# Performance work log

Measured on AMD Instinct MI355X. Metric: run time of the kernel, lower is better.

The kernel has to match this reference:

```python
import jax, jax.numpy as jnp
import numpy as np

B = 2048      # batch (number of event graphs)
NU = 128      # nodes in 'upstream' star graph per sample
ND = 128      # nodes in 'downstream' star graph per sample
FEAT = 10     # raw feature columns; fp[:, :7] used, column -3 (=7) is split flag
IN_DIM = 7    # state_dim + 1 + 2
HID = 64      # hidden1
TAU = 22      # tau_num
ALPHA = 0.2


def star_adj(n):
    # prepare_eg: edges[0,:]=1, symmetrized, diagonal zeroed -> star graph around node 0
    idx = jnp.arange(n)
    return (((idx[:, None] == 0) | (idx[None, :] == 0)) & (idx[:, None] != idx[None, :])).astype(jnp.float32)


def gat(h, W, a, adj, concat):
    # pyGAT GraphAttentionLayer (dropout=0): h [B,n,f], W [f,d], a [2d,1]
    d = W.shape[1]
    Wh = jnp.einsum('bnf,fd->bnd', h, W)                      # [B,n,d]
    e = Wh @ a[:d] + jnp.swapaxes(Wh @ a[d:], 1, 2)           # [B,n,n]
    e = jax.nn.leaky_relu(e, ALPHA)
    e = jnp.where(adj > 0, e, -9e15)
    att = jax.nn.softmax(e, axis=-1)
    hp = jnp.einsum('bnm,bmd->bnd', att, Wh)                  # [B,n,d]
    return jax.nn.elu(hp) if concat else hp


def setup_inputs() -> dict:
    key = jax.random.key(0)
    ks = jax.random.split(key, 12)
    fp = jax.random.normal(ks[0], (B, NU + ND, FEAT), dtype=jnp.float32)
    # column -3: first NU rows negative (u side), last ND rows positive (d side)
    fp = fp.at[:, :NU, FEAT - 3].set(-1.0)
    fp = fp.at[:, NU:, FEAT - 3].set(1.0)
    s = 0.1
    return {
        'fp': fp,
        'u_att_W': jax.random.normal(ks[1], (IN_DIM, HID), jnp.float32) * s,
        'u_att_a': jax.random.normal(ks[2], (2 * HID, 1), jnp.float32) * s,
        'u_out_W': jax.random.normal(ks[3], (HID, HID), jnp.float32) * s,
        'u_out_a': jax.random.normal(ks[4], (2 * HID, 1), jnp.float32) * s,
        'd_att_W': jax.random.normal(ks[5], (IN_DIM, HID), jnp.float32) * s,
        'd_att_a': jax.random.normal(ks[6], (2 * HID, 1), jnp.float32) * s,
        'd_out_W': jax.random.normal(ks[7], (HID, HID), jnp.float32) * s,
        'd_out_a': jax.random.normal(ks[8], (2 * HID, 1), jnp.float32) * s,
        'fc2_W': jax.random.normal(ks[9], (HID, TAU), jnp.float32) * s,
        'fc2_b': jax.random.normal(ks[10], (TAU,), jnp.float32) * s,
    }


def reference(fp, u_att_W, u_att_a, u_out_W, u_out_a,
              d_att_W, d_att_a, d_out_W, d_out_a, fc2_W, fc2_b):
    # static split by the sign of column -3 (fp is constructed so the first NU
    # rows have flag<=0 and the last ND rows have flag>=0, matching prepare_eg)
    u_x = fp[:, :NU, :IN_DIM]   # [B,NU,7]
    d_x = fp[:, NU:, :IN_DIM]   # [B,ND,7]
    u_adj = star_adj(NU)
    d_adj = star_adj(ND)
    # u_egat: 1 attention head (concat->elu) then out layer (no elu), sum over nodes
    u_h = gat(gat(u_x, u_att_W, u_att_a, u_adj, True), u_out_W, u_out_a, u_adj, False)
    u_g = jnp.sum(u_h, axis=1)  # [B,HID]
    d_h = gat(gat(d_x, d_att_W, d_att_a, d_adj, True), d_out_W, d_out_a, d_adj, False)
    d_g = jnp.sum(d_h, axis=1)  # [B,HID]
    a = jax.nn.relu((u_g + d_g) @ fc2_W + fc2_b)  # [B,TAU]
    # torch.sort result is discarded; forward returns W.clamp(0, 10)
    return jnp.clip(a, 0.0, 10.0)
```

## Files before the change

kernel.cpp:

```cpp
#include <hip/hip_runtime.h>
#include <math.h>

#define NB     2048
#define FEAT   10
#define IN_DIM 7
#define HID    64
#define TAU    22
#define ALPHA  0.2f

template <int CTRL>
__device__ __forceinline__ float dpp_mv(float x) {
    return __int_as_float(__builtin_amdgcn_update_dpp(
        0, __float_as_int(x), CTRL, 0xf, 0xf, true));
}

__device__ __forceinline__ float wave_sum64(float v) {
    v += dpp_mv<0xB1>(v);
    v += dpp_mv<0x4E>(v);
    v += dpp_mv<0x141>(v);
    v += dpp_mv<0x140>(v);
    v += dpp_mv<0x142>(v);
    v += dpp_mv<0x143>(v);
    return __int_as_float(__builtin_amdgcn_readlane(__float_as_int(v), 63));
}

__global__ __launch_bounds__(256) void gat_star_one(
    const float* __restrict__ fp,
    const float* __restrict__ uW1, const float* __restrict__ uA1,
    const float* __restrict__ uW2,
    const float* __restrict__ dW1, const float* __restrict__ dA1,
    const float* __restrict__ dW2,
    const float* __restrict__ fcW, const float* __restrict__ fcB,
    float* __restrict__ out)
{
    __shared__ float svs[4][16];
    __shared__ float vvs[4][HID];
    __shared__ float pts[4][HID];
    __shared__ float rrs[4][TAU];

    const int tid  = threadIdx.x;
    const int wave = tid >> 6;
    const int lane = tid & 63;
    const int it   = wave >> 1;
    const int half = wave & 1;
    const int item = blockIdx.x * 2 + it;

    const float* xbase = fp + (size_t)item * 256 * FEAT + half * 128 * FEAT;
    const float* pAp = xbase + lane * FEAT;
    const float* pBp = pAp + 64 * FEAT;
    const float2 a0 = *(const float2*)(pAp + 0);
    const float2 a1 = *(const float2*)(pAp + 2);
    const float2 a2 = *(const float2*)(pAp + 4);
    const float  a6 = pAp[6];
    const float2 b0 = *(const float2*)(pBp + 0);
    const float2 b1 = *(const float2*)(pBp + 2);
    const float2 b2 = *(const float2*)(pBp + 4);
    const float  b6 = pBp[6];
    const float4 x03 = *(const float4*)xbase;
    const float2 x45 = *(const float2*)(xbase + 4);
    const float  x6  = xbase[6];

    const float* W1 = half ? dW1 : uW1;
    const float* A1 = half ? dA1 : uA1;
    float w1c[IN_DIM];
    #pragma unroll
    for (int f = 0; f < IN_DIM; ++f) w1c[f] = W1[f * HID + lane];

    if (lane < 14) {
        const int sp = (lane >= IN_DIM) ? 1 : 0;
        const int f  = lane - sp * IN_DIM;
        const float* wr = W1 + f * HID;
        const float* av = A1 + sp * HID;
        float s0 = 0.f, s1 = 0.f, s2 = 0.f, s3 = 0.f;
        #pragma unroll
        for (int k = 0; k < HID; k += 4) {
            s0 = fmaf(wr[k + 0], av[k + 0], s0);
            s1 = fmaf(wr[k + 1], av[k + 1], s1);
            s2 = fmaf(wr[k + 2], av[k + 2], s2);
            s3 = fmaf(wr[k + 3], av[k + 3], s3);
        }
        svs[wave][sp * 8 + f] = (s0 + s1) + (s2 + s3);
    }
    __builtin_amdgcn_wave_barrier();

    float x0[IN_DIM], xA[IN_DIM], xB[IN_DIM];
    x0[0] = x03.x; x0[1] = x03.y; x0[2] = x03.z; x0[3] = x03.w;
    x0[4] = x45.x; x0[5] = x45.y; x0[6] = x6;
    xA[0] = a0.x; xA[1] = a0.y; xA[2] = a1.x; xA[3] = a1.y;
    xA[4] = a2.x; xA[5] = a2.y; xA[6] = a6;
    xB[0] = b0.x; xB[1] = b0.y; xB[2] = b1.x; xB[3] = b1.y;
    xB[4] = b2.x; xB[5] = b2.y; xB[6] = b6;

    float sv1[IN_DIM], sv2[IN_DIM];
    #pragma unroll
    for (int f = 0; f < IN_DIM; ++f) {
        sv1[f] = svs[wave][f];
        sv2[f] = svs[wave][8 + f];
    }

    float s1 = 0.f, sA = 0.f, sB = 0.f;
    #pragma unroll
    for (int f = 0; f < IN_DIM; ++f) {
        s1 = fmaf(x0[f], sv1[f], s1);
        sA = fmaf(xA[f], sv2[f], sA);
        sB = fmaf(xB[f], sv2[f], sB);
    }
    float eA = s1 + sA; eA = (eA >= 0.f) ? eA : ALPHA * eA;
    float eB = s1 + sB; eB = (eB >= 0.f) ? eB : ALPHA * eB;

    const float qA = (lane == 0) ? 0.f : __expf(eA);
    const float qB = __expf(eB);
    float c[8];
    #pragma unroll
    for (int f = 0; f < IN_DIM; ++f)
        c[f] = wave_sum64(fmaf(qA, xA[f], qB * xB[f]));
    c[7] = wave_sum64(qA + qB);
    const float inv = 1.0f / c[7];

    float h0 = 0.f, h1 = 0.f;
    #pragma unroll
    for (int f = 0; f < IN_DIM; ++f) {
        h0 = fmaf(c[f],  w1c[f], h0);
        h1 = fmaf(x0[f], w1c[f], h1);
    }
    h0 *= inv;
    h0 = (h0 > 0.f) ? h0 : (__expf(h0) - 1.f);
    h1 = (h1 > 0.f) ? h1 : (__expf(h1) - 1.f);
    vvs[wave][lane] = h1 + 127.f * h0;
    __builtin_amdgcn_wave_barrier();

    {
        const float* W2 = half ? dW2 : uW2;
        const float* v  = vvs[wave];
        float t0 = 0.f, t1 = 0.f, t2 = 0.f, t3 = 0.f;
        #pragma unroll
        for (int k = 0; k < HID; k += 4) {
            t0 = fmaf(v[k + 0], W2[(k + 0) * HID + lane], t0);
            t1 = fmaf(v[k + 1], W2[(k + 1) * HID + lane], t1);
            t2 = fmaf(v[k + 2], W2[(k + 2) * HID + lane], t2);
            t3 = fmaf(v[k + 3], W2[(k + 3) * HID + lane], t3);
        }
        pts[wave][lane] = (t0 + t1) + (t2 + t3);
    }
    __builtin_amdgcn_wave_barrier();

    {
        const float* p = pts[wave];
        int t = lane & 31; if (t > TAU - 1) t = TAU - 1;
        const int jb = lane & 32;
        float s0 = 0.f, s1_ = 0.f;
        #pragma unroll
        for (int jj = 0; jj < 32; jj += 2) {
            s0  = fmaf(p[jb + jj],     fcW[(jb + jj)     * TAU + t], s0);
            s1_ = fmaf(p[jb + jj + 1], fcW[(jb + jj + 1) * TAU + t], s1_);
        }
        float s = s0 + s1_;
        s += __shfl_xor(s, 32);
        if (lane < TAU) rrs[wave][lane] = s;
    }
    __syncthreads();

    if (half == 0 && lane < TAU) {
        float s = rrs[wave][lane] + rrs[wave + 1][lane] + fcB[lane];
        s = fminf(fmaxf(s, 0.f), 10.f);
        out[(size_t)item * TAU + lane] = s;
    }
}

extern "C" void kernel_launch(void* const* d_in, const int* in_sizes, int n_in,
                              void* d_out, int out_size, void* d_ws, size_t ws_size,
                              hipStream_t stream) {
    const float* fp  = (const float*)d_in[0];
    const float* uW1 = (const float*)d_in[1];
    const float* uA1 = (const float*)d_in[2];
    const float* uW2 = (const float*)d_in[3];
    const float* dW1 = (const float*)d_in[5];
    const float* dA1 = (const float*)d_in[6];
    const float* dW2 = (const float*)d_in[7];
    const float* fcW = (const float*)d_in[9];
    const float* fcB = (const float*)d_in[10];
    float* out = (float*)d_out;

    gat_star_one<<<NB / 2, 256, 0, stream>>>(fp, uW1, uA1, uW2,
                                             dW1, dA1, dW2, fcW, fcB, out);
}
```

Measured before the change: 16.09 us.

## Replace per-lane serial dot products with wave-parallel DPP reductions and split-k matvecs

Attention-vector projections (W1·a) were computed serially on 14 lanes through shared memory. They are now computed across all lanes with DPP wave reductions. The W2 matvec is restructured as split-k over four 16-lane rows using float4 weight loads plus cross-row shuffles. The fc2 projection is fused directly from registers with row-level DPP sums, which removes the intermediate shared buffer and its barrier. This trades long serial dependent load chains for more cross-lane reduction instructions.

```diff
diff --git a/kernel.cpp b/kernel.cpp
--- a/kernel.cpp
+++ b/kernel.cpp
@@ -14,11 +14,16 @@
         0, __float_as_int(x), CTRL, 0xf, 0xf, true));
 }
 
-__device__ __forceinline__ float wave_sum64(float v) {
+__device__ __forceinline__ float row_sum16(float v) {
     v += dpp_mv<0xB1>(v);
     v += dpp_mv<0x4E>(v);
     v += dpp_mv<0x141>(v);
     v += dpp_mv<0x140>(v);
+    return v;
+}
+
+__device__ __forceinline__ float wave_sum64(float v) {
+    v = row_sum16(v);
     v += dpp_mv<0x142>(v);
     v += dpp_mv<0x143>(v);
     return __int_as_float(__builtin_amdgcn_readlane(__float_as_int(v), 63));
@@ -33,9 +38,7 @@
     const float* __restrict__ fcW, const float* __restrict__ fcB,
     float* __restrict__ out)
 {
-    __shared__ float svs[4][16];
     __shared__ float vvs[4][HID];
-    __shared__ float pts[4][HID];
     __shared__ float rrs[4][TAU];
 
     const int tid  = threadIdx.x;
@@ -65,23 +68,15 @@
     float w1c[IN_DIM];
     #pragma unroll
     for (int f = 0; f < IN_DIM; ++f) w1c[f] = W1[f * HID + lane];
+    const float alo = A1[lane];
+    const float ahi = A1[HID + lane];
 
-    if (lane < 14) {
-        const int sp = (lane >= IN_DIM) ? 1 : 0;
-        const int f  = lane - sp * IN_DIM;
-        const float* wr = W1 + f * HID;
-        const float* av = A1 + sp * HID;
-        float s0 = 0.f, s1 = 0.f, s2 = 0.f, s3 = 0.f;
-        #pragma unroll
-        for (int k = 0; k < HID; k += 4) {
-            s0 = fmaf(wr[k + 0], av[k + 0], s0);
-            s1 = fmaf(wr[k + 1], av[k + 1], s1);
-            s2 = fmaf(wr[k + 2], av[k + 2], s2);
-            s3 = fmaf(wr[k + 3], av[k + 3], s3);
-        }
-        svs[wave][sp * 8 + f] = (s0 + s1) + (s2 + s3);
+    float sv1[IN_DIM], sv2[IN_DIM];
+    #pragma unroll
+    for (int f = 0; f < IN_DIM; ++f) {
+        sv1[f] = wave_sum64(w1c[f] * alo);
+        sv2[f] = wave_sum64(w1c[f] * ahi);
     }
-    __builtin_amdgcn_wave_barrier();
 
     float x0[IN_DIM], xA[IN_DIM], xB[IN_DIM];
     x0[0] = x03.x; x0[1] = x03.y; x0[2] = x03.z; x0[3] = x03.w;
@@ -90,13 +85,6 @@
     xA[4] = a2.x; xA[5] = a2.y; xA[6] = a6;
     xB[0] = b0.x; xB[1] = b0.y; xB[2] = b1.x; xB[3] = b1.y;
     xB[4] = b2.x; xB[5] = b2.y; xB[6] = b6;
-
-    float sv1[IN_DIM], sv2[IN_DIM];
-    #pragma unroll
-    for (int f = 0; f < IN_DIM; ++f) {
-        sv1[f] = svs[wave][f];
-        sv2[f] = svs[wave][8 + f];
-    }
 
     float s1 = 0.f, sA = 0.f, sB = 0.f;
     #pragma unroll
@@ -129,34 +117,47 @@
     vvs[wave][lane] = h1 + 127.f * h0;
     __builtin_amdgcn_wave_barrier();
 
-    {
-        const float* W2 = half ? dW2 : uW2;
-        const float* v  = vvs[wave];
-        float t0 = 0.f, t1 = 0.f, t2 = 0.f, t3 = 0.f;
-        #pragma unroll
-        for (int k = 0; k < HID; k += 4) {
-            t0 = fmaf(v[k + 0], W2[(k + 0) * HID + lane], t0);
-            t1 = fmaf(v[k + 1], W2[(k + 1) * HID + lane], t1);
-            t2 = fmaf(v[k + 2], W2[(k + 2) * HID + lane], t2);
-            t3 = fmaf(v[k + 3], W2[(k + 3) * HID + lane], t3);
+    const int jg = lane & 15;
+    const int kc = lane >> 4;
+    const float* W2 = half ? dW2 : uW2;
+    float t0 = 0.f, t1 = 0.f, t2 = 0.f, t3 = 0.f;
+    #pragma unroll
+    for (int kk = 0; kk < 16; ++kk) {
+        const int k = kc * 16 + kk;
+        const float vvk = vvs[wave][k];
+        const float4 w = *(const float4*)(W2 + k * HID + jg * 4);
+        t0 = fmaf(vvk, w.x, t0);
+        t1 = fmaf(vvk, w.y, t1);
+        t2 = fmaf(vvk, w.z, t2);
+        t3 = fmaf(vvk, w.w, t3);
+    }
+    t0 += __shfl_xor(t0, 16); t0 += __shfl_xor(t0, 32);
+    t1 += __shfl_xor(t1, 16); t1 += __shfl_xor(t1, 32);
+    t2 += __shfl_xor(t2, 16); t2 += __shfl_xor(t2, 32);
+    t3 += __shfl_xor(t3, 16); t3 += __shfl_xor(t3, 32);
+
+    const int tbase = kc * 6;
+    const int j4 = jg * 4;
+    float fs0 = 0.f, fs1 = 0.f, fs2 = 0.f, fs3 = 0.f, fs4 = 0.f, fs5 = 0.f;
+#define FC2_T(TT, DST)                                                        \
+    { const int t_ = tbase + (TT);                                            \
+      if (t_ < TAU) {                                                         \
+          float a_ = t0 * fcW[(j4 + 0) * TAU + t_];                           \
+          a_ = fmaf(t1, fcW[(j4 + 1) * TAU + t_], a_);                        \
+          a_ = fmaf(t2, fcW[(j4 + 2) * TAU + t_], a_);                        \
+          a_ = fmaf(t3, fcW[(j4 + 3) * TAU + t_], a_);                        \
+          DST = row_sum16(a_);                                                \
+      } }
+    FC2_T(0, fs0) FC2_T(1, fs1) FC2_T(2, fs2)
+    FC2_T(3, fs3) FC2_T(4, fs4) FC2_T(5, fs5)
+#undef FC2_T
+    if (jg < 6) {
+        const int t_ = tbase + jg;
+        if (t_ < TAU) {
+            float v_ = (jg == 0) ? fs0 : (jg == 1) ? fs1 : (jg == 2) ? fs2
+                     : (jg == 3) ? fs3 : (jg == 4) ? fs4 : fs5;
+            rrs[wave][t_] = v_;
         }
-        pts[wave][lane] = (t0 + t1) + (t2 + t3);
-    }
-    __builtin_amdgcn_wave_barrier();
-
-    {
-        const float* p = pts[wave];
-        int t = lane & 31; if (t > TAU - 1) t = TAU - 1;
-        const int jb = lane & 32;
-        float s0 = 0.f, s1_ = 0.f;
-        #pragma unroll
-        for (int jj = 0; jj < 32; jj += 2) {
-            s0  = fmaf(p[jb + jj],     fcW[(jb + jj)     * TAU + t], s0);
-            s1_ = fmaf(p[jb + jj + 1], fcW[(jb + jj + 1) * TAU + t], s1_);
-        }
-        float s = s0 + s1_;
-        s += __shfl_xor(s, 32);
-        if (lane < TAU) rrs[wave][lane] = s;
     }
     __syncthreads();
 
```

Measured after the change: 14.26 us. -11.4%, faster.
